# Kernel tuning notes

Measured on AMD Instinct MI355X. Metric: run time of the kernel, lower is better.

The kernel has to match this reference:

```python
import jax, jax.numpy as jnp
import numpy as np

N, E = 50000, 800000
X_DIM, EA_DIM, H, L = 128, 16, 128, 3
BN_EPS = 1e-5


def setup_inputs() -> dict:
    key = jax.random.key(0)
    ks = jax.random.split(key, 20)
    s = 0.02
    inp = {
        "x": jax.random.normal(ks[0], (N, X_DIM), jnp.float32),
        "edge_index": jax.random.randint(ks[1], (2, E), 0, N, jnp.int64),
        "batch": jnp.sort(jax.random.randint(ks[2], (N,), 0, 128, jnp.int64)),
        "edge_attr": jax.random.normal(ks[3], (E, EA_DIM), jnp.float32),
        "edge_atten": jax.random.uniform(ks[4], (E, 1), jnp.float32),
        # node_encoder2 and edge_encoder
        "W_enc": jax.random.normal(ks[5], (X_DIM, H), jnp.float32) * s,
        "b_enc": jnp.zeros((H,), jnp.float32),
        "W_ee": jax.random.normal(ks[6], (EA_DIM, H), jnp.float32) * s,
        "b_ee": jnp.zeros((H,), jnp.float32),
        # per-layer GINEConv params (stacked over layers)
        "eps": jnp.zeros((L,), jnp.float32),
        "W1": jax.random.normal(ks[7], (L, H, H), jnp.float32) * s,
        "b1": jnp.zeros((L, H), jnp.float32),
        "bn_gamma": jnp.ones((L, H), jnp.float32),
        "bn_beta": jnp.zeros((L, H), jnp.float32),
        "bn_mean": jnp.zeros((L, H), jnp.float32),
        "bn_var": jnp.ones((L, H), jnp.float32),
        "W2": jax.random.normal(ks[8], (L, H, H), jnp.float32) * s,
        "b2": jnp.zeros((L, H), jnp.float32),
    }
    return inp


def reference(x, edge_index, batch, edge_attr, edge_atten,
              W_enc, b_enc, W_ee, b_ee, eps,
              W1, b1, bn_gamma, bn_beta, bn_mean, bn_var, W2, b2):
    # node/edge encoders
    h = x @ W_enc + b_enc                      # [N, H]
    ea = edge_attr @ W_ee + b_ee               # [E, H]
    src, dst = edge_index[0], edge_index[1]
    n = h.shape[0]
    for i in range(L):
        # GINEConv message: relu(x_j + edge_attr) * edge_atten, scatter-add to dst
        m = jax.nn.relu(h[src] + ea) * edge_atten          # [E, H]
        aggr = jax.ops.segment_sum(m, dst, num_segments=n) # [N, H]
        z = (1.0 + eps[i]) * h + aggr
        # MLP: Linear -> BatchNorm(eval, running stats) -> ReLU -> Linear
        z = z @ W1[i] + b1[i]
        z = (z - bn_mean[i]) * jax.lax.rsqrt(bn_var[i] + BN_EPS) * bn_gamma[i] + bn_beta[i]
        z = jax.nn.relu(z)
        z = z @ W2[i] + b2[i]
        # outer relu; dropout is identity in eval mode
        h = jax.nn.relu(z)
    return h
```

## Files before the change

### kernel.cpp

```cpp
#include <hip/hip_runtime.h>
#include <hip/hip_fp16.h>
#include <cstdint>
#include <cstddef>


typedef _Float16 f16x8 __attribute__((ext_vector_type(8)));
typedef float    f32x4 __attribute__((ext_vector_type(4)));
typedef float    f32x2 __attribute__((ext_vector_type(2)));

__device__ inline uint32_t pack_fp8_pair(float a, float b) {
#if __has_builtin(__builtin_amdgcn_cvt_pk_fp8_f32)
    return (uint32_t)__builtin_amdgcn_cvt_pk_fp8_f32(a, b, 0, false) & 0xFFFFu;
#else
    auto enc = [](float x) -> uint32_t {
        uint32_t s = (x < 0.f) ? 0x80u : 0u;
        float ax = fabsf(x);
        if (!(ax >= 1.953125e-3f)) {
            int mi = (int)(ax * 512.f + 0.5f);
            if (mi > 7) mi = 7;
            return s | (uint32_t)mi;
        }
        ax = fminf(ax, 448.f);
        int e; float m = frexpf(ax, &e);
        int E = e - 1 + 7;
        int mi = (int)((m * 2.f - 1.f) * 8.f + 0.5f);
        if (mi == 8) { mi = 0; ++E; }
        if (E > 15 || (E == 15 && mi == 7)) { E = 15; mi = 6; }
        return s | ((uint32_t)E << 3) | (uint32_t)mi;
    };
    return enc(a) | (enc(b) << 8);
#endif
}

template <bool HIGH>
__device__ inline f32x2 unpack_fp8_pair(uint32_t w) {
#if __has_builtin(__builtin_amdgcn_cvt_pk_f32_fp8)
    return __builtin_amdgcn_cvt_pk_f32_fp8((int)w, HIGH);
#else
    auto dec = [](uint32_t v) -> float {
        uint32_t s = v >> 7, e = (v >> 3) & 0xF, m = v & 7;
        float r = (e == 0) ? ldexpf((float)m, -9)
                           : ldexpf(1.f + (float)m / 8.f, (int)e - 7);
        return s ? -r : r;
    };
    uint32_t b0 = HIGH ? ((w >> 16) & 0xFF) : (w & 0xFF);
    uint32_t b1 = HIGH ? ((w >> 24) & 0xFF) : ((w >> 8) & 0xFF);
    return (f32x2){dec(b0), dec(b1)};
#endif
}

template <class T>
__device__ inline auto add2_impl(T* p, T v, int)
    -> decltype(unsafeAtomicAdd(p, v), void()) {
    unsafeAtomicAdd(p, v);
}
template <class T>
__device__ inline void add2_impl(T* p, T v, long) {
    unsafeAtomicAdd(&p->x, v.x);
    unsafeAtomicAdd(&p->y, v.y);
}
__device__ inline void atomic_add2(float* p, float x, float y) {
    add2_impl(reinterpret_cast<float2*>(p), make_float2(x, y), 0);
}

__global__ void init_arrays(int* __restrict__ cnt, int N, int* __restrict__ eids, int S)
{
    int i = blockIdx.x * blockDim.x + threadIdx.x;
    const int st = gridDim.x * blockDim.x;
    for (int j = i; j < N; j += st) cnt[j] = 0;
    for (int j = i; j < S; j += st) eids[j] = -1;
}

__global__ void hist_kernel(const int* __restrict__ ei, int* __restrict__ cnt, int E)
{
    int i = blockIdx.x * blockDim.x + threadIdx.x;
    const int st = gridDim.x * blockDim.x;
    for (; i < E; i += st) atomicAdd(&cnt[ei[E + i]], 1);
}

__global__ __launch_bounds__(256) void scan_pass1(
    const int* __restrict__ cnt, int* __restrict__ bsum, int N)
{
    __shared__ int part[256];
    const int t = threadIdx.x;
    const int base = blockIdx.x * 1024 + t * 4;
    int s = 0;
#pragma unroll
    for (int j = 0; j < 4; ++j) {
        int idx = base + j;
        if (idx < N) { int v = cnt[idx]; s += v + (v & 1); }
    }
    part[t] = s;
    __syncthreads();
    for (int d = 128; d > 0; d >>= 1) {
        if (t < d) part[t] += part[t + d];
        __syncthreads();
    }
    if (t == 0) bsum[blockIdx.x] = part[0];
}

__global__ __launch_bounds__(256) void scan_pass2(
    int* __restrict__ bsum, int* __restrict__ off, int NB, int N)
{
    __shared__ int sb[1024];
    const int t = threadIdx.x;
    for (int i = t; i < NB; i += 256) sb[i] = bsum[i];
    __syncthreads();
    if (t == 0) {
        int run = 0;
        for (int i = 0; i < NB; ++i) { int v = sb[i]; sb[i] = run; run += v; }
        off[N] = run;
    }
    __syncthreads();
    for (int i = t; i < NB; i += 256) bsum[i] = sb[i];
}

__global__ __launch_bounds__(256) void scan_pass3(
    const int* __restrict__ cnt, const int* __restrict__ bsum,
    int* __restrict__ off, int* __restrict__ cur, int N)
{
    __shared__ int part[256];
    const int t = threadIdx.x;
    const int base = blockIdx.x * 1024 + t * 4;
    int pv[4]; int s = 0;
#pragma unroll
    for (int j = 0; j < 4; ++j) {
        int idx = base + j;
        int v = (idx < N) ? cnt[idx] : 0;
        pv[j] = v + (v & 1);
        s += pv[j];
    }
    part[t] = s;
    __syncthreads();
    for (int d = 1; d < 256; d <<= 1) {
        int x = (t >= d) ? part[t - d] : 0;
        __syncthreads();
        part[t] += x;
        __syncthreads();
    }
    int run = bsum[blockIdx.x] + part[t] - s;
#pragma unroll
    for (int j = 0; j < 4; ++j) {
        int idx = base + j;
        if (idx < N) { off[idx] = run; cur[idx] = run; }
        run += pv[j];
    }
}

__global__ void scatter_kernel(const int* __restrict__ ei, int* __restrict__ cur,
                               int* __restrict__ eids, int E)
{
    int i = blockIdx.x * blockDim.x + threadIdx.x;
    const int st = gridDim.x * blockDim.x;
    for (; i < E; i += st) {
        int pos = atomicAdd(&cur[ei[E + i]], 1);
        eids[pos] = i;
    }
}

__global__ void permute_sat(
    const int* __restrict__ ei, const float* __restrict__ eatten,
    const int* __restrict__ eids, const int* __restrict__ offN,
    float2* __restrict__ sat, int Scap)
{
    const int S = *offN;
    int i = blockIdx.x * blockDim.x + threadIdx.x;
    const int st = gridDim.x * blockDim.x;
    for (; i < S; i += st) {
        const int eid = eids[i];
        float2 v;
        if (eid >= 0) { v.x = __int_as_float(ei[eid]); v.y = eatten[eid]; }
        else          { v.x = __int_as_float(0);       v.y = 0.f; }
        sat[i] = v;
    }
}

__global__ __launch_bounds__(256) void eabuild_staged(
    const int* __restrict__ eids, const float* __restrict__ eattr,
    const float* __restrict__ W_ee, const float* __restrict__ b_ee,
    const int* __restrict__ offN, uint16_t* __restrict__ eab8, int Scap)
{
    __shared__ int   se[256];
    __shared__ float sattr[256 * 16];
    const int t = threadIdx.x;
    const int lane = t & 63;
    const int wv = t >> 6;
    const int c = lane * 2;

    const int S = *offN;
    const int base = blockIdx.x * 256;
    const int n = min(256, S - base);
    if (n <= 0) return;

    float2 w[16];
#pragma unroll
    for (int k = 0; k < 16; ++k) w[k] = *(const float2*)&W_ee[k * 128 + c];
    const float2 bv = *(const float2*)&b_ee[c];

    if (t < n) se[t] = eids[base + t];
    __syncthreads();

    float4* sa4 = (float4*)sattr;
    const float4* ea4 = (const float4*)eattr;
    for (int i = t; i < n * 4; i += 256) {
        const int row = i >> 2, part = i & 3;
        const int eid = se[row];
        sa4[i] = (eid >= 0) ? ea4[(size_t)eid * 4 + part]
                            : make_float4(0.f, 0.f, 0.f, 0.f);
    }
    __syncthreads();

    for (int slot = wv; slot < n; slot += 4) {
        const int gs = base + slot;
        uint32_t out = 0;
        if (se[slot] >= 0) {
            const float4* sr = (const float4*)&sattr[slot * 16];
            float4 e0 = sr[0], e1 = sr[1], e2 = sr[2], e3 = sr[3];
            const float ef[16] = {e0.x, e0.y, e0.z, e0.w, e1.x, e1.y, e1.z, e1.w,
                                  e2.x, e2.y, e2.z, e2.w, e3.x, e3.y, e3.z, e3.w};
            float d0 = bv.x, d1 = bv.y;
#pragma unroll
            for (int k = 0; k < 16; ++k) {
                d0 = fmaf(ef[k], w[k].x, d0);
                d1 = fmaf(ef[k], w[k].y, d1);
            }
            out = pack_fp8_pair(d0, d1);
        }
        eab8[(size_t)(gs >> 1) * 128 + lane * 2 + (gs & 1)] = (uint16_t)out;
    }
}

__global__ void prepack_w(const float* __restrict__ W1, const float* __restrict__ W2,
                          const float* __restrict__ Wenc,
                          _Float16* __restrict__ Wpk, int L)
{
    int tid = blockIdx.x * blockDim.x + threadIdx.x;
    const int total = (2 * L + 1) * 32 * 64;
    if (tid >= total) return;
    const int lane = tid & 63;
    const int f = (tid >> 6) & 31;
    const int lm = tid >> 11;
    const int kb = f >> 3, tc = f & 7;
    const float* src = (lm < L) ? (W1 + (size_t)lm * 16384)
                    : (lm < 2 * L) ? (W2 + (size_t)(lm - L) * 16384)
                    : Wenc;
    _Float16* dst = Wpk + ((size_t)lm * 32 + f) * 512 + lane * 8;
#pragma unroll
    for (int i = 0; i < 8; ++i) {
        const int k = kb * 32 + (lane >> 4) * 8 + i;
        const int col = tc * 16 + (lane & 15);
        dst[i] = (_Float16)src[k * 128 + col];
    }
}

__global__ void cvt_f16(const float* __restrict__ x, _Float16* __restrict__ y, int n8)
{
    int i = blockIdx.x * blockDim.x + threadIdx.x;
    const int st = gridDim.x * blockDim.x;
    for (; i < n8; i += st) {
        float4 a = ((const float4*)x)[2 * i];
        float4 b = ((const float4*)x)[2 * i + 1];
        f16x8 v = {(_Float16)a.x, (_Float16)a.y, (_Float16)a.z, (_Float16)a.w,
                   (_Float16)b.x, (_Float16)b.y, (_Float16)b.z, (_Float16)b.w};
        ((f16x8*)y)[i] = v;
    }
}

__global__ __launch_bounds__(256) void enc_mfma(
    const _Float16* __restrict__ x16, const _Float16* __restrict__ Wpk,
    const float* __restrict__ bias, _Float16* __restrict__ h16, int n)
{
    const int t = threadIdx.x;
    const int lane = t & 63;
    const int w = t >> 6;
    const int row0 = blockIdx.x * 64;
    const int lr = lane & 15;
    const int lg = lane >> 4;

    f32x4 acc[8];
#pragma unroll
    for (int tc = 0; tc < 8; ++tc) acc[tc] = (f32x4){0.f, 0.f, 0.f, 0.f};
    const int arow = min(row0 + w * 16 + lr, n - 1);
#pragma unroll
    for (int kb = 0; kb < 4; ++kb) {
        f16x8 a = *(const f16x8*)&x16[(size_t)arow * 128 + kb * 32 + lg * 8];
#pragma unroll
        for (int tc = 0; tc < 8; ++tc) {
            f16x8 b = *(const f16x8*)&Wpk[((kb * 8 + tc) * 64 + lane) * 8];
            acc[tc] = __builtin_amdgcn_mfma_f32_16x16x32_f16(a, b, acc[tc], 0, 0, 0);
        }
    }
#pragma unroll
    for (int tc = 0; tc < 8; ++tc) {
        const int col = tc * 16 + lr;
        const float bb = bias[col];
#pragma unroll
        for (int j = 0; j < 4; ++j) {
            const int row = row0 + w * 16 + lg * 4 + j;
            if (row < n)
                h16[(size_t)row * 128 + col] = (_Float16)(acc[tc][j] + bb);
        }
    }
}

__global__ __launch_bounds__(256) void agg_f8(
    const _Float16* __restrict__ h16, const float2* __restrict__ sat,
    const uint32_t* __restrict__ eab8, const int* __restrict__ off,
    _Float16* __restrict__ z16, const float* __restrict__ eps, int layer, int N)
{
    const int t = threadIdx.x;
    const int v = blockIdx.x * 4 + (t >> 6);
    if (v >= N) return;
    const int lane = t & 63;
    const int c = lane * 2;

    const int e0 = off[v], e1 = off[v + 1];
    float a0 = 0.f, a1 = 0.f;
    int e = e0;
    for (; e + 8 <= e1; e += 8) {
        float4 sa[2];
        sa[0] = *(const float4*)&sat[e];
        sa[1] = *(const float4*)&sat[e + 2];
        float4 sb[2];
        sb[0] = *(const float4*)&sat[e + 4];
        sb[1] = *(const float4*)&sat[e + 6];
        uint32_t eb[4];
#pragma unroll
        for (int j = 0; j < 4; ++j)
            eb[j] = eab8[(size_t)((e >> 1) + j) * 64 + lane];
        uint32_t hv[8];
        hv[0] = *(const uint32_t*)&h16[(size_t)__float_as_int(sa[0].x) * 128 + c];
        hv[1] = *(const uint32_t*)&h16[(size_t)__float_as_int(sa[0].z) * 128 + c];
        hv[2] = *(const uint32_t*)&h16[(size_t)__float_as_int(sa[1].x) * 128 + c];
        hv[3] = *(const uint32_t*)&h16[(size_t)__float_as_int(sa[1].z) * 128 + c];
        hv[4] = *(const uint32_t*)&h16[(size_t)__float_as_int(sb[0].x) * 128 + c];
        hv[5] = *(const uint32_t*)&h16[(size_t)__float_as_int(sb[0].z) * 128 + c];
        hv[6] = *(const uint32_t*)&h16[(size_t)__float_as_int(sb[1].x) * 128 + c];
        hv[7] = *(const uint32_t*)&h16[(size_t)__float_as_int(sb[1].z) * 128 + c];
#pragma unroll
        for (int j = 0; j < 4; ++j) {
            const float4 s4 = (j < 2) ? sa[j] : sb[j - 2];
            f32x2 ev = unpack_fp8_pair<false>(eb[j]);
            f32x2 od = unpack_fp8_pair<true>(eb[j]);
            __half2 h0 = *reinterpret_cast<const __half2*>(&hv[2 * j]);
            __half2 h1 = *reinterpret_cast<const __half2*>(&hv[2 * j + 1]);
            a0 += fmaxf(__half2float(__low2half(h0))  + ev[0], 0.f) * s4.y;
            a1 += fmaxf(__half2float(__high2half(h0)) + ev[1], 0.f) * s4.y;
            a0 += fmaxf(__half2float(__low2half(h1))  + od[0], 0.f) * s4.w;
            a1 += fmaxf(__half2float(__high2half(h1)) + od[1], 0.f) * s4.w;
        }
    }
    for (; e < e1; e += 2) {
        float4 sa = *(const float4*)&sat[e];
        uint32_t eb = eab8[(size_t)(e >> 1) * 64 + lane];
        uint32_t hv0 = *(const uint32_t*)&h16[(size_t)__float_as_int(sa.x) * 128 + c];
        uint32_t hv1 = *(const uint32_t*)&h16[(size_t)__float_as_int(sa.z) * 128 + c];
        f32x2 ev = unpack_fp8_pair<false>(eb);
        f32x2 od = unpack_fp8_pair<true>(eb);
        __half2 h0 = *reinterpret_cast<const __half2*>(&hv0);
        __half2 h1 = *reinterpret_cast<const __half2*>(&hv1);
        a0 += fmaxf(__half2float(__low2half(h0))  + ev[0], 0.f) * sa.y;
        a1 += fmaxf(__half2float(__high2half(h0)) + ev[1], 0.f) * sa.y;
        a0 += fmaxf(__half2float(__low2half(h1))  + od[0], 0.f) * sa.w;
        a1 += fmaxf(__half2float(__high2half(h1)) + od[1], 0.f) * sa.w;
    }

    const float sc = 1.0f + eps[layer];
    uint32_t hvv = *(const uint32_t*)&h16[(size_t)v * 128 + c];
    __half2 hh = *reinterpret_cast<const __half2*>(&hvv);
    float zx = fmaf(sc, __half2float(__low2half(hh)), a0);
    float zy = fmaf(sc, __half2float(__high2half(hh)), a1);
    __half2 zz = __floats2half2_rn(zx, zy);
    *reinterpret_cast<__half2*>(&z16[(size_t)v * 128 + c]) = zz;
}

__global__ __launch_bounds__(256) void mlp_mfma(
    const _Float16* __restrict__ z16,
    const _Float16* __restrict__ W1pk, const float* __restrict__ b1,
    const float* __restrict__ gam, const float* __restrict__ bet,
    const float* __restrict__ mu, const float* __restrict__ var,
    const _Float16* __restrict__ W2pk, const float* __restrict__ b2,
    _Float16* __restrict__ h16out, float* __restrict__ H, int last, int n)
{
    __shared__ _Float16 Yt[64][136];
    const int t = threadIdx.x;
    const int lane = t & 63;
    const int w = t >> 6;
    const int row0 = blockIdx.x * 64;
    const int lr = lane & 15;
    const int lg = lane >> 4;

    f32x4 acc[8];
#pragma unroll
    for (int tc = 0; tc < 8; ++tc) acc[tc] = (f32x4){0.f, 0.f, 0.f, 0.f};
    const int arow = min(row0 + w * 16 + lr, n - 1);
#pragma unroll
    for (int kb = 0; kb < 4; ++kb) {
        f16x8 a = *(const f16x8*)&z16[(size_t)arow * 128 + kb * 32 + lg * 8];
#pragma unroll
        for (int tc = 0; tc < 8; ++tc) {
            f16x8 b = *(const f16x8*)&W1pk[((kb * 8 + tc) * 64 + lane) * 8];
            acc[tc] = __builtin_amdgcn_mfma_f32_16x16x32_f16(a, b, acc[tc], 0, 0, 0);
        }
    }
#pragma unroll
    for (int tc = 0; tc < 8; ++tc) {
        const int col = tc * 16 + lr;
        const float s  = gam[col] * rsqrtf(var[col] + 1e-5f);
        const float sh = bet[col] - mu[col] * s;
        const float bb = b1[col];
#pragma unroll
        for (int j = 0; j < 4; ++j) {
            float y = fmaxf(fmaf(acc[tc][j] + bb, s, sh), 0.f);
            Yt[w * 16 + lg * 4 + j][col] = (_Float16)y;
        }
    }
    __syncthreads();

#pragma unroll
    for (int tc = 0; tc < 8; ++tc) acc[tc] = (f32x4){0.f, 0.f, 0.f, 0.f};
#pragma unroll
    for (int kb = 0; kb < 4; ++kb) {
        f16x8 a = *(const f16x8*)&Yt[w * 16 + lr][kb * 32 + lg * 8];
#pragma unroll
        for (int tc = 0; tc < 8; ++tc) {
            f16x8 b = *(const f16x8*)&W2pk[((kb * 8 + tc) * 64 + lane) * 8];
            acc[tc] = __builtin_amdgcn_mfma_f32_16x16x32_f16(a, b, acc[tc], 0, 0, 0);
        }
    }
#pragma unroll
    for (int tc = 0; tc < 8; ++tc) {
        const int col = tc * 16 + lr;
        const float bb = b2[col];
#pragma unroll
        for (int j = 0; j < 4; ++j) {
            const int row = row0 + w * 16 + lg * 4 + j;
            if (row < n) {
                const float o = fmaxf(acc[tc][j] + bb, 0.f);
                if (last) H[(size_t)row * 128 + col] = o;
                else      h16out[(size_t)row * 128 + col] = (_Float16)o;
            }
        }
    }
}

__global__ __launch_bounds__(512, 4) void gemm_enc(
    const float* __restrict__ A, const float* __restrict__ W,
    const float* __restrict__ bias, float* __restrict__ H, int n)
{
    __shared__ float At[64][128];
    __shared__ float Wb[2][16][128];
    const int t = threadIdx.x;
    const int tx = t & 31, ty = t >> 5;

    const int row0 = blockIdx.x * 64;
    const int nrows = min(64, n - row0);
    const int lim = nrows * 32;
    const float4* A4 = (const float4*)(A + (size_t)row0 * 128);
    float4* At4 = (float4*)&At[0][0];
#pragma unroll
    for (int i = 0; i < 4; ++i) {
        int idx = t + 512 * i;
        if (idx < lim) At4[idx] = A4[idx];
    }
    const float4* W4 = (const float4*)W;
    ((float4*)&Wb[0][0][0])[t] = W4[t];
    __syncthreads();

    float acc[4][4] = {};
    for (int c = 0; c < 8; ++c) {
        const int buf = c & 1;
        float4 wnext;
        if (c < 7) wnext = W4[(c + 1) * 512 + t];
#pragma unroll
        for (int g = 0; g < 4; ++g) {
            float4 w4[4];
#pragma unroll
            for (int kk = 0; kk < 4; ++kk) w4[kk] = *(const float4*)&Wb[buf][g * 4 + kk][tx * 4];
#pragma unroll
            for (int r = 0; r < 4; ++r) {
                float4 a = *(const float4*)&At[ty * 4 + r][c * 16 + g * 4];
                float ar[4] = {a.x, a.y, a.z, a.w};
#pragma unroll
                for (int kk = 0; kk < 4; ++kk) {
                    acc[r][0] = fmaf(ar[kk], w4[kk].x, acc[r][0]);
                    acc[r][1] = fmaf(ar[kk], w4[kk].y, acc[r][1]);
                    acc[r][2] = fmaf(ar[kk], w4[kk].z, acc[r][2]);
                    acc[r][3] = fmaf(ar[kk], w4[kk].w, acc[r][3]);
                }
            }
        }
        if (c < 7) ((float4*)&Wb[buf ^ 1][0][0])[t] = wnext;
        __syncthreads();
    }

    const int c0 = tx * 4;
    float bvv[4];
#pragma unroll
    for (int c = 0; c < 4; ++c) bvv[c] = bias[c0 + c];
#pragma unroll
    for (int r = 0; r < 4; ++r) {
        int row = row0 + ty * 4 + r;
        if (row < n) {
            float4 o;
            o.x = acc[r][0] + bvv[0]; o.y = acc[r][1] + bvv[1];
            o.z = acc[r][2] + bvv[2]; o.w = acc[r][3] + bvv[3];
            *(float4*)&H[(size_t)row * 128 + c0] = o;
        }
    }
}

__global__ void scale_init(const float* __restrict__ h, float* __restrict__ z,
                           const float* __restrict__ eps, int layer, int n4)
{
    const float s = 1.0f + eps[layer];
    int i = blockIdx.x * blockDim.x + threadIdx.x;
    const int stride = gridDim.x * blockDim.x;
    const float4* h4 = (const float4*)h;
    float4* z4 = (float4*)z;
    for (; i < n4; i += stride) {
        float4 v = h4[i];
        v.x *= s; v.y *= s; v.z *= s; v.w *= s;
        z4[i] = v;
    }
}

__global__ __launch_bounds__(256) void edge_atomic(
    const float* __restrict__ h, const int* __restrict__ ei,
    const float* __restrict__ eattr, const float* __restrict__ eatten,
    const float* __restrict__ W_ee, const float* __restrict__ b_ee,
    float* __restrict__ Z, int E)
{
    __shared__ float Wee[16][128];
    __shared__ float bee[128];
    const int t = threadIdx.x;
    const float4* We4 = (const float4*)W_ee;
    float4* Ws4 = (float4*)&Wee[0][0];
#pragma unroll
    for (int i = 0; i < 2; ++i) Ws4[t + 256 * i] = We4[t + 256 * i];
    if (t < 128) bee[t] = b_ee[t];
    __syncthreads();

    const int lane = t & 63;
    const int c = lane * 2;
    const long wid = (long)blockIdx.x * 4 + (t >> 6);
    const long nw = (long)gridDim.x * 4;
    for (long e = wid; e < E; e += nw) {
        const int src = ei[e];
        const int dst = ei[E + e];
        const float att = eatten[e];
        union { float4 v4[4]; float f[16]; } ea;
        const float4* eap = (const float4*)(eattr + e * 16);
        ea.v4[0] = eap[0]; ea.v4[1] = eap[1]; ea.v4[2] = eap[2]; ea.v4[3] = eap[3];
        float2 hv = *(const float2*)&h[(size_t)src * 128 + c];
        float e0 = bee[c], e1 = bee[c + 1];
#pragma unroll
        for (int k = 0; k < 16; ++k) {
            float2 w = *(const float2*)&Wee[k][c];
            e0 = fmaf(ea.f[k], w.x, e0);
            e1 = fmaf(ea.f[k], w.y, e1);
        }
        float m0 = fmaxf(hv.x + e0, 0.f) * att;
        float m1 = fmaxf(hv.y + e1, 0.f) * att;
        atomic_add2(&Z[(size_t)dst * 128 + c], m0, m1);
    }
}

__global__ __launch_bounds__(512, 4) void gemm_mlp(
    const float* __restrict__ Z,
    const float* __restrict__ W1, const float* __restrict__ b1,
    const float* __restrict__ gam, const float* __restrict__ bet,
    const float* __restrict__ mu, const float* __restrict__ var,
    const float* __restrict__ W2, const float* __restrict__ b2,
    float* __restrict__ H, int n)
{
    __shared__ float At[64][128];
    __shared__ float Wb[2][16][128];
    const int t = threadIdx.x;
    const int tx = t & 31, ty = t >> 5;

    const int row0 = blockIdx.x * 64;
    const int nrows = min(64, n - row0);
    const int lim = nrows * 32;
    const float4* Z4 = (const float4*)(Z + (size_t)row0 * 128);
    float4* At4 = (float4*)&At[0][0];
#pragma unroll
    for (int i = 0; i < 4; ++i) {
        int idx = t + 512 * i;
        if (idx < lim) At4[idx] = Z4[idx];
    }
    const float4* W14 = (const float4*)W1;
    ((float4*)&Wb[0][0][0])[t] = W14[t];
    __syncthreads();

    float acc[4][4] = {};
    for (int c = 0; c < 8; ++c) {
        const int buf = c & 1;
        float4 wnext;
        if (c < 7) wnext = W14[(c + 1) * 512 + t];
#pragma unroll
        for (int g = 0; g < 4; ++g) {
            float4 w4[4];
#pragma unroll
            for (int kk = 0; kk < 4; ++kk) w4[kk] = *(const float4*)&Wb[buf][g * 4 + kk][tx * 4];
#pragma unroll
            for (int r = 0; r < 4; ++r) {
                float4 a = *(const float4*)&At[ty * 4 + r][c * 16 + g * 4];
                float ar[4] = {a.x, a.y, a.z, a.w};
#pragma unroll
                for (int kk = 0; kk < 4; ++kk) {
                    acc[r][0] = fmaf(ar[kk], w4[kk].x, acc[r][0]);
                    acc[r][1] = fmaf(ar[kk], w4[kk].y, acc[r][1]);
                    acc[r][2] = fmaf(ar[kk], w4[kk].z, acc[r][2]);
                    acc[r][3] = fmaf(ar[kk], w4[kk].w, acc[r][3]);
                }
            }
        }
        if (c < 7) ((float4*)&Wb[buf ^ 1][0][0])[t] = wnext;
        __syncthreads();
    }

    const int c0 = tx * 4;
    const float4* W24 = (const float4*)W2;
    float4 w2pre = W24[t];
    {
        float b1v[4], scv[4], shv[4];
#pragma unroll
        for (int cl = 0; cl < 4; ++cl) {
            b1v[cl] = b1[c0 + cl];
            float s = gam[c0 + cl] * rsqrtf(var[c0 + cl] + 1e-5f);
            scv[cl] = s;
            shv[cl] = bet[c0 + cl] - mu[c0 + cl] * s;
        }
#pragma unroll
        for (int r = 0; r < 4; ++r) {
            float4 y;
            y.x = fmaxf(fmaf(acc[r][0] + b1v[0], scv[0], shv[0]), 0.f);
            y.y = fmaxf(fmaf(acc[r][1] + b1v[1], scv[1], shv[1]), 0.f);
            y.z = fmaxf(fmaf(acc[r][2] + b1v[2], scv[2], shv[2]), 0.f);
            y.w = fmaxf(fmaf(acc[r][3] + b1v[3], scv[3], shv[3]), 0.f);
            *(float4*)&At[ty * 4 + r][c0] = y;
            acc[r][0] = 0.f; acc[r][1] = 0.f; acc[r][2] = 0.f; acc[r][3] = 0.f;
        }
    }
    ((float4*)&Wb[0][0][0])[t] = w2pre;
    __syncthreads();

    for (int c = 0; c < 8; ++c) {
        const int buf = c & 1;
        float4 wnext;
        if (c < 7) wnext = W24[(c + 1) * 512 + t];
#pragma unroll
        for (int g = 0; g < 4; ++g) {
            float4 w4[4];
#pragma unroll
            for (int kk = 0; kk < 4; ++kk) w4[kk] = *(const float4*)&Wb[buf][g * 4 + kk][tx * 4];
#pragma unroll
            for (int r = 0; r < 4; ++r) {
                float4 a = *(const float4*)&At[ty * 4 + r][c * 16 + g * 4];
                float ar[4] = {a.x, a.y, a.z, a.w};
#pragma unroll
                for (int kk = 0; kk < 4; ++kk) {
                    acc[r][0] = fmaf(ar[kk], w4[kk].x, acc[r][0]);
                    acc[r][1] = fmaf(ar[kk], w4[kk].y, acc[r][1]);
                    acc[r][2] = fmaf(ar[kk], w4[kk].z, acc[r][2]);
                    acc[r][3] = fmaf(ar[kk], w4[kk].w, acc[r][3]);
                }
            }
        }
        if (c < 7) ((float4*)&Wb[buf ^ 1][0][0])[t] = wnext;
        __syncthreads();
    }

    float b2v[4];
#pragma unroll
    for (int cl = 0; cl < 4; ++cl) b2v[cl] = b2[c0 + cl];
#pragma unroll
    for (int r = 0; r < 4; ++r) {
        int row = row0 + ty * 4 + r;
        if (row < n) {
            float4 o;
            o.x = fmaxf(acc[r][0] + b2v[0], 0.f);
            o.y = fmaxf(acc[r][1] + b2v[1], 0.f);
            o.z = fmaxf(acc[r][2] + b2v[2], 0.f);
            o.w = fmaxf(acc[r][3] + b2v[3], 0.f);
            *(float4*)&H[(size_t)row * 128 + c0] = o;
        }
    }
}

extern "C" void kernel_launch(void* const* d_in, const int* in_sizes, int n_in,
                              void* d_out, int out_size, void* d_ws, size_t ws_size,
                              hipStream_t stream)
{
    const float* x      = (const float*)d_in[0];
    const int*   ei     = (const int*)d_in[1];
    const float* eattr  = (const float*)d_in[3];
    const float* eatten = (const float*)d_in[4];
    const float* W_enc  = (const float*)d_in[5];
    const float* b_enc  = (const float*)d_in[6];
    const float* W_ee   = (const float*)d_in[7];
    const float* b_ee   = (const float*)d_in[8];
    const float* eps    = (const float*)d_in[9];
    const float* W1     = (const float*)d_in[10];
    const float* b1     = (const float*)d_in[11];
    const float* gam    = (const float*)d_in[12];
    const float* bet    = (const float*)d_in[13];
    const float* mu     = (const float*)d_in[14];
    const float* var    = (const float*)d_in[15];
    const float* W2     = (const float*)d_in[16];
    const float* b2     = (const float*)d_in[17];

    const int N = in_sizes[0] / 128;
    const int E = in_sizes[1] / 2;
    const int L = in_sizes[9];
    const int Scap = E + N;

    float* hout = (float*)d_out;

    char* p = (char*)d_ws;
    _Float16* z16 = (_Float16*)p;       p += ((size_t)N * 128 * 2 + 255) & ~(size_t)255;
    _Float16* h16 = (_Float16*)p;       p += ((size_t)N * 128 * 2 + 255) & ~(size_t)255;
    int* off  = (int*)p;                p += 4 * (size_t)(N + 1);
    int* cur  = (int*)p;                p += 4 * (size_t)N;
    int* cnt  = (int*)p;                p += 4 * (size_t)N;
    int* bsum = (int*)p;                p += 4 * 1024;
    int* eids = (int*)p;                p += 4 * (size_t)Scap;
    p = (char*)(((uintptr_t)p + 255) & ~(uintptr_t)255);
    float2* sat = (float2*)p;           p += 8 * (size_t)Scap;
    p = (char*)(((uintptr_t)p + 255) & ~(uintptr_t)255);
    uint16_t* eab8 = (uint16_t*)p;      p += 256 * (size_t)((Scap + 1) / 2);
    p = (char*)(((uintptr_t)p + 255) & ~(uintptr_t)255);
    _Float16* Wpk = (_Float16*)p;       p += (2 * (size_t)L + 1) * 32 * 512 * 2;
    const size_t need_main = (size_t)(p - (char*)d_ws);

    const bool use_main = ws_size >= need_main;
    const int tiles = (N + 63) / 64;
    const int NB = (N + 1023) / 1024;

    if (use_main) {
        _Float16* x16 = z16;

        init_arrays<<<1024, 256, 0, stream>>>(cnt, N, eids, Scap);
        hist_kernel<<<1024, 256, 0, stream>>>(ei, cnt, E);
        scan_pass1<<<NB, 256, 0, stream>>>(cnt, bsum, N);
        scan_pass2<<<1, 256, 0, stream>>>(bsum, off, NB, N);
        scan_pass3<<<NB, 256, 0, stream>>>(cnt, bsum, off, cur, N);
        scatter_kernel<<<1024, 256, 0, stream>>>(ei, cur, eids, E);
        permute_sat<<<1024, 256, 0, stream>>>(ei, eatten, eids, off + N, sat, Scap);
        eabuild_staged<<<(Scap + 255) / 256, 256, 0, stream>>>(
            eids, eattr, W_ee, b_ee, off + N, eab8, Scap);
        prepack_w<<<((2 * L + 1) * 32 * 64 + 255) / 256, 256, 0, stream>>>(
            W1, W2, W_enc, Wpk, L);

        cvt_f16<<<2048, 256, 0, stream>>>(x, x16, N * 128 / 8);
        enc_mfma<<<tiles, 256, 0, stream>>>(
            x16, Wpk + (size_t)(2 * L) * 32 * 512, b_enc, h16, N);

        for (int i = 0; i < L; ++i) {
            agg_f8<<<(N + 3) / 4, 256, 0, stream>>>(
                h16, sat, (const uint32_t*)eab8, off, z16, eps, i, N);
            mlp_mfma<<<tiles, 256, 0, stream>>>(
                z16,
                Wpk + (size_t)i * 32 * 512, b1 + i * 128,
                gam + i * 128, bet + i * 128, mu + i * 128, var + i * 128,
                Wpk + (size_t)(L + i) * 32 * 512, b2 + i * 128,
                h16, hout, (i == L - 1) ? 1 : 0, N);
        }
        return;
    }

    float* zbuf = (float*)d_ws;
    float* h = hout;
    gemm_enc<<<tiles, 512, 0, stream>>>(x, W_enc, b_enc, h, N);
    for (int i = 0; i < L; ++i) {
        scale_init<<<2048, 256, 0, stream>>>(h, zbuf, eps, i, N * 128 / 4);
        edge_atomic<<<2048, 256, 0, stream>>>(h, ei, eattr, eatten, W_ee, b_ee, zbuf, E);
        gemm_mlp<<<tiles, 512, 0, stream>>>(
            zbuf, W1 + (size_t)i * 128 * 128, b1 + i * 128,
            gam + i * 128, bet + i * 128, mu + i * 128, var + i * 128,
            W2 + (size_t)i * 128 * 128, b2 + i * 128,
            h, N);
    }
}
```

Baseline: 423.3 us.

## Fuse edge permutation into MFMA-based edge encoder build

```diff
diff --git a/kernel.cpp b/kernel.cpp
--- a/kernel.cpp
+++ b/kernel.cpp
@@ -158,33 +158,21 @@
     }
 }
 
-__global__ void permute_sat(
+__global__ __launch_bounds__(256) void eabuild_mfma(
+    const int* __restrict__ eids, const float* __restrict__ eattr,
     const int* __restrict__ ei, const float* __restrict__ eatten,
-    const int* __restrict__ eids, const int* __restrict__ offN,
+    const float* __restrict__ W_ee, const float* __restrict__ b_ee,
+    const int* __restrict__ offN, uint32_t* __restrict__ eab32,
     float2* __restrict__ sat, int Scap)
 {
-    const int S = *offN;
-    int i = blockIdx.x * blockDim.x + threadIdx.x;
-    const int st = gridDim.x * blockDim.x;
-    for (; i < S; i += st) {
-        const int eid = eids[i];
-        float2 v;
-        if (eid >= 0) { v.x = __int_as_float(ei[eid]); v.y = eatten[eid]; }
-        else          { v.x = __int_as_float(0);       v.y = 0.f; }
-        sat[i] = v;
-    }
-}
-
-__global__ __launch_bounds__(256) void eabuild_staged(
-    const int* __restrict__ eids, const float* __restrict__ eattr,
-    const float* __restrict__ W_ee, const float* __restrict__ b_ee,
-    const int* __restrict__ offN, uint16_t* __restrict__ eab8, int Scap)
-{
-    __shared__ int   se[256];
-    __shared__ float sattr[256 * 16];
+    __shared__ int      se[256];
+    __shared__ _Float16 sattr16[256][16];
+    __shared__ float    eaL[4][16][132];
     const int t = threadIdx.x;
     const int lane = t & 63;
-    const int wv = t >> 6;
+    const int w = t >> 6;
+    const int lr = lane & 15;
+    const int lg = lane >> 4;
     const int c = lane * 2;
 
     const int S = *offN;
@@ -192,41 +180,71 @@
     const int n = min(256, S - base);
     if (n <= 0) return;
 
-    float2 w[16];
-#pragma unroll
-    for (int k = 0; k < 16; ++k) w[k] = *(const float2*)&W_ee[k * 128 + c];
+    f16x8 bfrag[8];
+#pragma unroll
+    for (int tc = 0; tc < 8; ++tc) {
+        f16x8 b = {};
+        if (lg < 2) {
+#pragma unroll
+            for (int i = 0; i < 8; ++i)
+                b[i] = (_Float16)W_ee[(lg * 8 + i) * 128 + tc * 16 + lr];
+        }
+        bfrag[tc] = b;
+    }
     const float2 bv = *(const float2*)&b_ee[c];
 
     if (t < n) se[t] = eids[base + t];
     __syncthreads();
 
-    float4* sa4 = (float4*)sattr;
-    const float4* ea4 = (const float4*)eattr;
-    for (int i = t; i < n * 4; i += 256) {
-        const int row = i >> 2, part = i & 3;
-        const int eid = se[row];
-        sa4[i] = (eid >= 0) ? ea4[(size_t)eid * 4 + part]
-                            : make_float4(0.f, 0.f, 0.f, 0.f);
-    }
-    __syncthreads();
-
-    for (int slot = wv; slot < n; slot += 4) {
-        const int gs = base + slot;
-        uint32_t out = 0;
-        if (se[slot] >= 0) {
-            const float4* sr = (const float4*)&sattr[slot * 16];
-            float4 e0 = sr[0], e1 = sr[1], e2 = sr[2], e3 = sr[3];
-            const float ef[16] = {e0.x, e0.y, e0.z, e0.w, e1.x, e1.y, e1.z, e1.w,
-                                  e2.x, e2.y, e2.z, e2.w, e3.x, e3.y, e3.z, e3.w};
-            float d0 = bv.x, d1 = bv.y;
-#pragma unroll
-            for (int k = 0; k < 16; ++k) {
-                d0 = fmaf(ef[k], w[k].x, d0);
-                d1 = fmaf(ef[k], w[k].y, d1);
-            }
-            out = pack_fp8_pair(d0, d1);
-        }
-        eab8[(size_t)(gs >> 1) * 128 + lane * 2 + (gs & 1)] = (uint16_t)out;
+    if (t < n) {
+        const int eid = se[t];
+        float2 v;
+        f16x8 lo = {}, hi = {};
+        if (eid >= 0) {
+            v.x = __int_as_float(ei[eid]); v.y = eatten[eid];
+            const float4* ep = (const float4*)(eattr + (size_t)eid * 16);
+            float4 e0 = ep[0], e1 = ep[1], e2 = ep[2], e3 = ep[3];
+            lo = (f16x8){(_Float16)e0.x, (_Float16)e0.y, (_Float16)e0.z, (_Float16)e0.w,
+                         (_Float16)e1.x, (_Float16)e1.y, (_Float16)e1.z, (_Float16)e1.w};
+            hi = (f16x8){(_Float16)e2.x, (_Float16)e2.y, (_Float16)e2.z, (_Float16)e2.w,
+                         (_Float16)e3.x, (_Float16)e3.y, (_Float16)e3.z, (_Float16)e3.w};
+        } else {
+            v.x = __int_as_float(0); v.y = 0.f;
+        }
+        sat[base + t] = v;
+        *(f16x8*)&sattr16[t][0] = lo;
+        *(f16x8*)&sattr16[t][8] = hi;
+    } else {
+        *(f16x8*)&sattr16[t][0] = (f16x8){};
+        *(f16x8*)&sattr16[t][8] = (f16x8){};
+    }
+    __syncthreads();
+
+#pragma unroll
+    for (int k = 0; k < 4; ++k) {
+        const int tb = w * 64 + k * 16;
+        if (tb >= n) break;
+        f16x8 af = {};
+        if (lg < 2)
+            af = *(const f16x8*)&sattr16[tb + lr][lg * 8];
+#pragma unroll
+        for (int tc = 0; tc < 8; ++tc) {
+            f32x4 acc = __builtin_amdgcn_mfma_f32_16x16x32_f16(
+                af, bfrag[tc], (f32x4){0.f, 0.f, 0.f, 0.f}, 0, 0, 0);
+#pragma unroll
+            for (int j = 0; j < 4; ++j)
+                eaL[w][lg * 4 + j][tc * 16 + lr] = acc[j];
+        }
+#pragma unroll
+        for (int pp = 0; pp < 8; ++pp) {
+            const int s0 = tb + 2 * pp;
+            if (s0 >= n) break;
+            float2 ea0 = *(const float2*)&eaL[w][2 * pp][c];
+            float2 ea1 = *(const float2*)&eaL[w][2 * pp + 1][c];
+            uint32_t p0 = pack_fp8_pair(ea0.x + bv.x, ea0.y + bv.y);
+            uint32_t p1 = pack_fp8_pair(ea1.x + bv.x, ea1.y + bv.y);
+            eab32[(size_t)((base + s0) >> 1) * 64 + lane] = p0 | (p1 << 16);
+        }
     }
 }
 
@@ -729,7 +747,7 @@
     p = (char*)(((uintptr_t)p + 255) & ~(uintptr_t)255);
     float2* sat = (float2*)p;           p += 8 * (size_t)Scap;
     p = (char*)(((uintptr_t)p + 255) & ~(uintptr_t)255);
-    uint16_t* eab8 = (uint16_t*)p;      p += 256 * (size_t)((Scap + 1) / 2);
+    uint32_t* eab32 = (uint32_t*)p;     p += 256 * (size_t)((Scap + 1) / 2);
     p = (char*)(((uintptr_t)p + 255) & ~(uintptr_t)255);
     _Float16* Wpk = (_Float16*)p;       p += (2 * (size_t)L + 1) * 32 * 512 * 2;
     const size_t need_main = (size_t)(p - (char*)d_ws);
@@ -747,9 +765,8 @@
         scan_pass2<<<1, 256, 0, stream>>>(bsum, off, NB, N);
         scan_pass3<<<NB, 256, 0, stream>>>(cnt, bsum, off, cur, N);
         scatter_kernel<<<1024, 256, 0, stream>>>(ei, cur, eids, E);
-        permute_sat<<<1024, 256, 0, stream>>>(ei, eatten, eids, off + N, sat, Scap);
-        eabuild_staged<<<(Scap + 255) / 256, 256, 0, stream>>>(
-            eids, eattr, W_ee, b_ee, off + N, eab8, Scap);
+        eabuild_mfma<<<(Scap + 255) / 256, 256, 0, stream>>>(
+            eids, eattr, ei, eatten, W_ee, b_ee, off + N, eab32, sat, Scap);
         prepack_w<<<((2 * L + 1) * 32 * 64 + 255) / 256, 256, 0, stream>>>(
             W1, W2, W_enc, Wpk, L);
 
@@ -759,7 +776,7 @@
 
         for (int i = 0; i < L; ++i) {
             agg_f8<<<(N + 3) / 4, 256, 0, stream>>>(
-                h16, sat, (const uint32_t*)eab8, off, z16, eps, i, N);
+                h16, sat, eab32, off, z16, eps, i, N);
             mlp_mfma<<<tiles, 256, 0, stream>>>(
                 z16,
                 Wpk + (size_t)i * 32 * 512, b1 + i * 128,
```

New measurement: 408.9 us. 3.4% less time.
